# Optimization experiments

Hardware: AMD Instinct MI355X
Metric: run time of the kernel (lower is better)

## Reference

```python
import jax, jax.numpy as jnp
import numpy as np

HEADS = 16
EPS = 1e-6


def setup_inputs() -> dict:
    key = jax.random.key(0)
    k1, k2, k3 = jax.random.split(key, 3)
    B, N, C = 4, 4096, 1024
    x = jax.random.normal(k1, (B, N, C), dtype=jnp.float32)
    w_qkv = jax.random.normal(k2, (3 * C, C), dtype=jnp.float32) * (C ** -0.5)
    w_out = jax.random.normal(k3, (C, C), dtype=jnp.float32) * (C ** -0.5)
    b_out = jnp.zeros((C,), dtype=jnp.float32)
    return {"x": x, "w_qkv": w_qkv, "w_out": w_out, "b_out": b_out}


def reference(x, w_qkv, w_out, b_out):
    B, N, C = x.shape
    H = HEADS
    D = C // H
    scale = D ** -0.25

    qkv = x @ w_qkv.T  # [B, N, 3C]
    q, k, v = jnp.split(qkv, 3, axis=-1)

    def heads(t):  # [B, N, C] -> [B, H, N, D]
        return t.reshape(B, N, H, D).transpose(0, 2, 1, 3)

    q, k, v = heads(q), heads(k), heads(v)

    feat = lambda t: jax.nn.elu(t) + 1.0
    q = feat(q) * scale
    k = feat(k) * scale

    kv = jnp.einsum('bhnd,bhne->bhde', k, v)      # [B, H, D, D]
    out = jnp.einsum('bhnd,bhde->bhne', q, kv)    # [B, H, N, D]
    k_sum = k.sum(axis=2)                          # [B, H, D]
    denom = jnp.einsum('bhnd,bhd->bhn', q, k_sum)  # [B, H, N]
    out = out / (denom[..., None] + EPS)

    out = out.transpose(0, 2, 1, 3).reshape(B, N, C)
    return out @ w_out.T + b_out
```

## Files before the change

### kernel.cpp

```cpp
#include <hip/hip_runtime.h>
#include <hip/hip_bf16.h>
#include <cmath>


typedef __bf16 bf16_t;
typedef __attribute__((ext_vector_type(8))) __bf16 bf16x8;
typedef __attribute__((ext_vector_type(4))) __bf16 bf16x4;
typedef __attribute__((ext_vector_type(4))) float f32x4;
typedef __attribute__((ext_vector_type(8))) float f32x8;

#define MFMA16(a, b, c) __builtin_amdgcn_mfma_f32_16x16x32_bf16((a), (b), (c), 0, 0, 0)

#define LDS_PITCH 72

__device__ __forceinline__ f32x4 zf4() { f32x4 z; z[0] = 0.f; z[1] = 0.f; z[2] = 0.f; z[3] = 0.f; return z; }

__device__ __forceinline__ float feat(float x) { return x > 0.f ? x + 1.f : expf(x); }

__device__ __forceinline__ void gld_lds16(const bf16_t* src, bf16_t* dst)
{
    __builtin_amdgcn_global_load_lds(
        (__attribute__((address_space(1))) void*)const_cast<bf16_t*>(src),
        (__attribute__((address_space(3))) void*)dst, 16, 0, 0);
}

template <int NR>
__device__ __forceinline__ void stage_async(const bf16_t* g, int ld, bf16_t* lds, int tid)
{
    const int w = tid >> 6, l = tid & 63;
    constexpr int CALLS = NR >> 5;
#pragma unroll
    for (int p = 0; p < CALLS; ++p) {
        const int chunk = w * CALLS + p;
        const int gidx = chunk * 64 + l;
        const int row = gidx >> 3;
        const int cp = gidx & 7;
        const int c = cp ^ (row & 7);
        gld_lds16(g + row * ld + c * 8, lds + chunk * 512);
    }
}

__device__ __forceinline__ bf16x8 read_frag_sw(const bf16_t* lds, int row, int cg)
{
    const int sw = cg ^ (row & 7);
    return *(const bf16x8*)(lds + row * 64 + sw * 8);
}

__global__ __launch_bounds__(256) void cvt3_kernel(
    const float* __restrict__ x, bf16_t* __restrict__ xb,
    const float* __restrict__ wq, bf16_t* __restrict__ wqb,
    const float* __restrict__ wo, bf16_t* __restrict__ wob)
{
    const int bid = blockIdx.x;
    const float* src;
    bf16_t* dst;
    int base;
    if (bid < 8192)      { src = x;  dst = xb;  base = bid; }
    else if (bid < 9728) { src = wq; dst = wqb; base = bid - 8192; }
    else                 { src = wo; dst = wob; base = bid - 9728; }
    const size_t idx = ((size_t)base * 256 + threadIdx.x) * 8;
    f32x8 f = *(const f32x8*)(src + idx);
    bf16x8 v;
#pragma unroll
    for (int t = 0; t < 8; ++t) v[t] = (bf16_t)f[t];
    *(bf16x8*)(dst + idx) = v;
}

template <int MODE>
__global__ __launch_bounds__(256, 4) void gemm_bt_kernel(
    const bf16_t* __restrict__ A, const bf16_t* __restrict__ B, int K,
    void* __restrict__ out0, bf16_t* __restrict__ out1, bf16_t* __restrict__ out2,
    const float* __restrict__ bias)
{
    __shared__ __align__(16) bf16_t As[128 * 64];
    __shared__ __align__(16) bf16_t Bs[128 * 64];
    const int tid = threadIdx.x;
    const int l = tid & 63, w = tid >> 6;
    const int wm = w >> 1, wn = w & 1;
    const int quad = l >> 4, r16 = l & 15;

    const int nwg = gridDim.x * gridDim.y;
    const int cpx = nwg >> 3;
    const int bid = blockIdx.y * gridDim.x + blockIdx.x;
    const int swz = (bid & 7) * cpx + (bid >> 3);
    const int m0 = (swz / gridDim.x) * 128;
    const int n0 = (swz % gridDim.x) * 128;

    f32x4 acc[4][4];
#pragma unroll
    for (int i = 0; i < 4; ++i)
#pragma unroll
        for (int j = 0; j < 4; ++j) acc[i][j] = zf4();

    const bf16_t* Ab = A + (size_t)m0 * K;
    const bf16_t* Bb = B + (size_t)n0 * K;

    for (int k0 = 0; k0 < K; k0 += 64) {
        stage_async<128>(Ab + k0, K, As, tid);
        stage_async<128>(Bb + k0, K, Bs, tid);
        __syncthreads();
#pragma unroll
        for (int ks = 0; ks < 2; ++ks) {
            const int cg = ks * 4 + quad;
            bf16x8 af[4], bfr[4];
#pragma unroll
            for (int i = 0; i < 4; ++i) af[i] = read_frag_sw(As, wm * 64 + i * 16 + r16, cg);
#pragma unroll
            for (int j = 0; j < 4; ++j) bfr[j] = read_frag_sw(Bs, wn * 64 + j * 16 + r16, cg);
#pragma unroll
            for (int i = 0; i < 4; ++i)
#pragma unroll
                for (int j = 0; j < 4; ++j)
                    acc[i][j] = MFMA16(af[i], bfr[j], acc[i][j]);
        }
        __syncthreads();
    }

    const float scale = 0.3535533905932738f;
#pragma unroll
    for (int i = 0; i < 4; ++i) {
        const int mbase = m0 + wm * 64 + i * 16 + quad * 4;
#pragma unroll
        for (int j = 0; j < 4; ++j) {
            const int col = n0 + wn * 64 + j * 16 + r16;
            if (MODE == 1) {
                float* yp = (float*)out0;
                const float bb = bias[col];
#pragma unroll
                for (int r = 0; r < 4; ++r)
                    yp[(size_t)(mbase + r) * 1024 + col] = acc[i][j][r] + bb;
            } else {
                const int part = col >> 10;
                const int cc = col & 1023;
                const int hh = (mbase >> 12) * 16 + (cc >> 6);
                const int d = cc & 63;
                const int ntok = mbase & 4095;
                if (part == 0) {
                    bf16_t* qp = (bf16_t*)out0 + ((size_t)hh * 4096 + ntok) * 64 + d;
#pragma unroll
                    for (int r = 0; r < 4; ++r)
                        qp[(size_t)r * 64] = (bf16_t)(feat(acc[i][j][r]) * scale);
                } else {
                    bf16_t* tp = (part == 1 ? out1 : out2) + ((size_t)hh * 64 + d) * 4096 + ntok;
                    bf16x4 pk;
#pragma unroll
                    for (int r = 0; r < 4; ++r) {
                        float v = acc[i][j][r];
                        if (part == 1) v = feat(v) * scale;
                        pk[r] = (bf16_t)v;
                    }
                    *(bf16x4*)tp = pk;
                }
            }
        }
    }
}

__global__ __launch_bounds__(256) void kv_partial_kernel(
    const bf16_t* __restrict__ KT, const bf16_t* __restrict__ VT,
    float* __restrict__ kvp, float* __restrict__ ksp_out)
{
    const int tid = threadIdx.x;
    const int l = tid & 63, w = tid >> 6;
    const int quad = l >> 4, r16 = l & 15;
    const int hh = blockIdx.x;
    const int ksp = blockIdx.y;
    const bf16_t* kb = KT + (size_t)hh * 64 * 4096 + ksp * 256 + quad * 8;
    const bf16_t* vb = VT + (size_t)hh * 64 * 4096 + ksp * 256 + quad * 8;
    const bf16_t* vrow = vb + (size_t)(w * 16 + r16) * 4096;

    bf16x8 ones;
#pragma unroll
    for (int t = 0; t < 8; ++t) ones[t] = (bf16_t)1.0f;

    f32x4 acc[4], accks[4];
#pragma unroll
    for (int j = 0; j < 4; ++j) { acc[j] = zf4(); accks[j] = zf4(); }

#pragma unroll
    for (int kk = 0; kk < 8; ++kk) {
        const int off = kk * 32;
        const bf16x8 af = *(const bf16x8*)(vrow + off);
        bf16x8 bk[4];
#pragma unroll
        for (int j = 0; j < 4; ++j)
            bk[j] = *(const bf16x8*)(kb + (size_t)(j * 16 + r16) * 4096 + off);
#pragma unroll
        for (int j = 0; j < 4; ++j) acc[j] = MFMA16(af, bk[j], acc[j]);
        if (w == 0) {
#pragma unroll
            for (int j = 0; j < 4; ++j) accks[j] = MFMA16(ones, bk[j], accks[j]);
        }
    }

    float* ob = kvp + (size_t)(hh * 16 + ksp) * 4096;
    const int ebase = w * 16 + quad * 4;
#pragma unroll
    for (int j = 0; j < 4; ++j)
#pragma unroll
        for (int r = 0; r < 4; ++r)
            ob[(ebase + r) * 64 + j * 16 + r16] = acc[j][r];

    if (w == 0 && quad == 0) {
        float* kso = ksp_out + (size_t)(hh * 16 + ksp) * 64;
#pragma unroll
        for (int j = 0; j < 4; ++j) kso[j * 16 + r16] = accks[j][0];
    }
}

__global__ __launch_bounds__(256, 2) void attn_out_kernel(
    const bf16_t* __restrict__ Q, const float* __restrict__ kvp, const float* __restrict__ ksp,
    bf16_t* __restrict__ att)
{
    __shared__ __align__(16) bf16_t kvT[64 * LDS_PITCH];
    __shared__ __align__(16) bf16_t ksb[64];
    const int tid = threadIdx.x;
    const int l = tid & 63, w = tid >> 6;
    const int quad = l >> 4, r16 = l & 15;
    const int hh = blockIdx.x;
    const int b = hh >> 4, h = hh & 15;
    const int mt = blockIdx.y;

    {
        const int e = tid >> 2, d0 = (tid & 3) * 16;
        const float* kvph = kvp + (size_t)hh * 16 * 4096 + e * 64 + d0;
        f32x4 s[4];
#pragma unroll
        for (int q4 = 0; q4 < 4; ++q4) s[q4] = *(const f32x4*)(kvph + q4 * 4);
#pragma unroll
        for (int p = 1; p < 16; ++p)
#pragma unroll
            for (int q4 = 0; q4 < 4; ++q4) s[q4] += *(const f32x4*)(kvph + p * 4096 + q4 * 4);
        bf16x8 o0, o1;
#pragma unroll
        for (int r = 0; r < 4; ++r) {
            o0[r] = (bf16_t)s[0][r]; o0[4 + r] = (bf16_t)s[1][r];
            o1[r] = (bf16_t)s[2][r]; o1[4 + r] = (bf16_t)s[3][r];
        }
        *(bf16x8*)(kvT + e * LDS_PITCH + d0)     = o0;
        *(bf16x8*)(kvT + e * LDS_PITCH + d0 + 8) = o1;
        if (tid < 64) {
            const float* kp = ksp + (size_t)hh * 16 * 64 + tid;
            float ks = 0.f;
#pragma unroll
            for (int p = 0; p < 16; ++p) ks += kp[p * 64];
            ksb[tid] = (bf16_t)ks;
        }
    }
    __syncthreads();

    f32x4 acc[4][4];
    f32x4 dacc[4];
#pragma unroll
    for (int i = 0; i < 4; ++i) {
        dacc[i] = zf4();
#pragma unroll
        for (int j = 0; j < 4; ++j) acc[i][j] = zf4();
    }

    const int m0w = mt * 256 + w * 64;
    const bf16_t* qb = Q + (size_t)hh * 4096 * 64;
#pragma unroll
    for (int ks = 0; ks < 2; ++ks) {
        bf16x8 kf = *(const bf16x8*)(ksb + ks * 32 + quad * 8);
        if (r16 != 0) {
#pragma unroll
            for (int t = 0; t < 8; ++t) kf[t] = (bf16_t)0.f;
        }
        bf16x8 bfr[4];
#pragma unroll
        for (int j = 0; j < 4; ++j)
            bfr[j] = *(const bf16x8*)(kvT + (j * 16 + r16) * LDS_PITCH + ks * 32 + quad * 8);
#pragma unroll
        for (int i = 0; i < 4; ++i) {
            const bf16_t* qp = qb + (size_t)(m0w + i * 16 + r16) * 64 + ks * 32 + quad * 8;
            const bf16x8 af = *(const bf16x8*)qp;
            dacc[i] = MFMA16(af, kf, dacc[i]);
#pragma unroll
            for (int j = 0; j < 4; ++j) acc[i][j] = MFMA16(af, bfr[j], acc[i][j]);
        }
    }

#pragma unroll
    for (int i = 0; i < 4; ++i) {
        float den[4];
#pragma unroll
        for (int r = 0; r < 4; ++r)
            den[r] = __shfl(dacc[i][r], l & 48) + 1e-6f;
#pragma unroll
        for (int j = 0; j < 4; ++j) {
            const size_t colb = (size_t)h * 64 + j * 16 + r16;
#pragma unroll
            for (int r = 0; r < 4; ++r) {
                const int ntok = m0w + i * 16 + quad * 4 + r;
                att[((size_t)b * 4096 + ntok) * 1024 + colb] = (bf16_t)(acc[i][j][r] / den[r]);
            }
        }
    }
}

extern "C" void kernel_launch(void* const* d_in, const int* in_sizes, int n_in,
                              void* d_out, int out_size, void* d_ws, size_t ws_size,
                              hipStream_t stream)
{
    const float* x    = (const float*)d_in[0];
    const float* wqkv = (const float*)d_in[1];
    const float* wout = (const float*)d_in[2];
    const float* bout = (const float*)d_in[3];
    float* y = (float*)d_out;

    char* ws = (char*)d_ws;
    bf16_t* xb    = (bf16_t*)ws;
    bf16_t* wqkvb = (bf16_t*)(ws + (size_t)32 * 1048576);
    bf16_t* woutb = (bf16_t*)(ws + (size_t)38 * 1048576);
    bf16_t* Q     = (bf16_t*)(ws + (size_t)40 * 1048576);
    bf16_t* KT    = (bf16_t*)(ws + (size_t)72 * 1048576);
    bf16_t* VT    = (bf16_t*)(ws + (size_t)104 * 1048576);
    float* kvp    = (float*)ws;
    float* ksp    = (float*)(ws + (size_t)16 * 1048576);
    bf16_t* att   = KT;

    cvt3_kernel<<<10240, 256, 0, stream>>>(x, xb, wqkv, wqkvb, wout, woutb);

    gemm_bt_kernel<0><<<dim3(24, 128), 256, 0, stream>>>(xb, wqkvb, 1024, Q, KT, VT, nullptr);
    kv_partial_kernel<<<dim3(64, 16), 256, 0, stream>>>(KT, VT, kvp, ksp);
    attn_out_kernel<<<dim3(64, 16), 256, 0, stream>>>(Q, kvp, ksp, att);
    gemm_bt_kernel<1><<<dim3(8, 128), 256, 0, stream>>>(att, woutb, 1024, y, nullptr, nullptr, bout);
}
```

Before: 336.3 us.

## Stage transposed K/V epilogue through LDS for coalesced global stores; drop tile swizzle

The QKV GEMM epilogue for the K and V parts now writes the accumulator tile transposed into a padded LDS buffer, then each thread copies contiguous 128-byte token rows to global memory with 16-byte vector stores. Previously each lane wrote scattered 8-byte chunks into the transposed layout. This targets the uncoalesced write cost of the transposed K/V layout. It also removes the workgroup index swizzle and uses plain blockIdx mapping, which may change L2 reuse, and enlarges the LDS allocation, which could affect occupancy.

```diff
diff --git a/kernel.cpp b/kernel.cpp
--- a/kernel.cpp
+++ b/kernel.cpp
@@ -12,6 +12,7 @@
 #define MFMA16(a, b, c) __builtin_amdgcn_mfma_f32_16x16x32_bf16((a), (b), (c), 0, 0, 0)
 
 #define LDS_PITCH 72
+#define TP_PITCH 132
 
 __device__ __forceinline__ f32x4 zf4() { f32x4 z; z[0] = 0.f; z[1] = 0.f; z[2] = 0.f; z[3] = 0.f; return z; }
 
@@ -72,19 +73,15 @@
     void* __restrict__ out0, bf16_t* __restrict__ out1, bf16_t* __restrict__ out2,
     const float* __restrict__ bias)
 {
-    __shared__ __align__(16) bf16_t As[128 * 64];
-    __shared__ __align__(16) bf16_t Bs[128 * 64];
+    __shared__ __align__(16) bf16_t smem[128 * TP_PITCH];
+    bf16_t* As = smem;
+    bf16_t* Bs = smem + 8192;
     const int tid = threadIdx.x;
     const int l = tid & 63, w = tid >> 6;
     const int wm = w >> 1, wn = w & 1;
     const int quad = l >> 4, r16 = l & 15;
-
-    const int nwg = gridDim.x * gridDim.y;
-    const int cpx = nwg >> 3;
-    const int bid = blockIdx.y * gridDim.x + blockIdx.x;
-    const int swz = (bid & 7) * cpx + (bid >> 3);
-    const int m0 = (swz / gridDim.x) * 128;
-    const int n0 = (swz % gridDim.x) * 128;
+    const int m0 = blockIdx.y * 128;
+    const int n0 = blockIdx.x * 128;
 
     f32x4 acc[4][4];
 #pragma unroll
@@ -117,31 +114,46 @@
     }
 
     const float scale = 0.3535533905932738f;
-#pragma unroll
-    for (int i = 0; i < 4; ++i) {
-        const int mbase = m0 + wm * 64 + i * 16 + quad * 4;
-#pragma unroll
-        for (int j = 0; j < 4; ++j) {
-            const int col = n0 + wn * 64 + j * 16 + r16;
-            if (MODE == 1) {
+    if (MODE == 1) {
+#pragma unroll
+        for (int i = 0; i < 4; ++i) {
+            const int mbase = m0 + wm * 64 + i * 16 + quad * 4;
+#pragma unroll
+            for (int j = 0; j < 4; ++j) {
+                const int col = n0 + wn * 64 + j * 16 + r16;
                 float* yp = (float*)out0;
                 const float bb = bias[col];
 #pragma unroll
                 for (int r = 0; r < 4; ++r)
                     yp[(size_t)(mbase + r) * 1024 + col] = acc[i][j][r] + bb;
-            } else {
-                const int part = col >> 10;
-                const int cc = col & 1023;
-                const int hh = (mbase >> 12) * 16 + (cc >> 6);
-                const int d = cc & 63;
-                const int ntok = mbase & 4095;
-                if (part == 0) {
+            }
+        }
+    } else {
+        const int part = n0 >> 10;
+        if (part == 0) {
+#pragma unroll
+            for (int i = 0; i < 4; ++i) {
+                const int mbase = m0 + wm * 64 + i * 16 + quad * 4;
+#pragma unroll
+                for (int j = 0; j < 4; ++j) {
+                    const int col = n0 + wn * 64 + j * 16 + r16;
+                    const int cc = col & 1023;
+                    const int hh = (mbase >> 12) * 16 + (cc >> 6);
+                    const int d = cc & 63;
+                    const int ntok = mbase & 4095;
                     bf16_t* qp = (bf16_t*)out0 + ((size_t)hh * 4096 + ntok) * 64 + d;
 #pragma unroll
                     for (int r = 0; r < 4; ++r)
                         qp[(size_t)r * 64] = (bf16_t)(feat(acc[i][j][r]) * scale);
-                } else {
-                    bf16_t* tp = (part == 1 ? out1 : out2) + ((size_t)hh * 64 + d) * 4096 + ntok;
+                }
+            }
+        } else {
+#pragma unroll
+            for (int i = 0; i < 4; ++i) {
+                const int tokb = wm * 64 + i * 16 + quad * 4;
+#pragma unroll
+                for (int j = 0; j < 4; ++j) {
+                    const int colc = wn * 64 + j * 16 + r16;
                     bf16x4 pk;
 #pragma unroll
                     for (int r = 0; r < 4; ++r) {
@@ -149,9 +161,19 @@
                         if (part == 1) v = feat(v) * scale;
                         pk[r] = (bf16_t)v;
                     }
-                    *(bf16x4*)tp = pk;
+                    *(bf16x4*)(smem + colc * TP_PITCH + tokb) = pk;
                 }
             }
+            __syncthreads();
+            bf16_t* basep = (part == 1 ? out1 : out2);
+            const int b = m0 >> 12, tokb = m0 & 4095;
+            const int row = tid >> 1, off = (tid & 1) * 64;
+            const int cc = (n0 & 1023) + row;
+            bf16_t* dst = basep + ((size_t)(b * 16 + (cc >> 6)) * 64 + (cc & 63)) * 4096 + tokb + off;
+            const bf16_t* srcl = smem + row * TP_PITCH + off;
+#pragma unroll
+            for (int c8 = 0; c8 < 8; ++c8)
+                *(bf16x8*)(dst + c8 * 8) = *(const bf16x8*)(srcl + c8 * 8);
         }
     }
 }
```

After: 352.4 us. +4.8%, slower.
